# Kernel tuning notes

Measured on AMD Instinct MI355X. Metric: run time of the kernel, lower is better.

Reference implementation:

```python
import jax, jax.numpy as jnp
import numpy as np

HEADS = 4
ATTN_MODE = 'strided'
LOCAL_ATTN_CTX = 32
BLOCKSIZE = 32


def strided_transpose(x, n_ctx, local_attn_ctx):
    # [n, t, e] -> [n, bT_ctx, local, e] -> [n, local, bT_ctx, e] -> [n, t, e]
    bT_ctx = n_ctx // local_attn_ctx
    n, t, e = x.shape
    x = x.reshape(n, bT_ctx, local_attn_ctx, e)
    x = jnp.transpose(x, (0, 2, 1, 3))
    return x.reshape(n, t, e)


def setup_inputs() -> dict:
    key = jax.random.key(0)
    kq, kk, kv = jax.random.split(key, 3)
    shape = (2, 4096, 1024)
    return {
        'q': jax.random.normal(kq, shape, dtype=jnp.float32),
        'k': jax.random.normal(kk, shape, dtype=jnp.float32),
        'v': jax.random.normal(kv, shape, dtype=jnp.float32),
    }


def reference(q, k, v):
    n_ctx = q.shape[1]
    if ATTN_MODE == 'strided':
        bT_ctx = n_ctx // LOCAL_ATTN_CTX
        assert bT_ctx % BLOCKSIZE == 0
        q = strided_transpose(q, n_ctx, LOCAL_ATTN_CTX)
        k = strided_transpose(k, n_ctx, LOCAL_ATTN_CTX)
        v = strided_transpose(v, n_ctx, LOCAL_ATTN_CTX)
    n_state = q.shape[-1] // HEADS
    scale = 1.0 / np.sqrt(n_state)
    w = jnp.einsum('nte,nse->nts', q, k)            # [n, t, t] full scores
    w = jax.nn.softmax(w * scale, axis=-1)
    a = jnp.einsum('nts,nse->nte', w, v)
    if ATTN_MODE == 'strided':
        n, t, e = a.shape
        bT_ctx = n_ctx // LOCAL_ATTN_CTX
        a = a.reshape(n, LOCAL_ATTN_CTX, bT_ctx, e)
        a = jnp.transpose(a, (0, 2, 1, 3))
        a = a.reshape(n, t, e)
    return a
```

## Files before the change

kernel.cpp:

```cpp
#include <hip/hip_runtime.h>

using short8  = __attribute__((ext_vector_type(8))) short;
using ushort8 = __attribute__((ext_vector_type(8))) unsigned short;
using f32x4   = __attribute__((ext_vector_type(4))) float;

#define T 4096
#define E 1024
#define NB 2
#define BM 128
#define BN 128
#define BK 32
#define TILE_ELEMS (BM * BK)
#define TILE_A_W   (256 * BK)

__device__ __forceinline__ unsigned short f2bf(float f) {
    unsigned int u = __builtin_bit_cast(unsigned int, f);
    u = (u + 0x7FFFu + ((u >> 16) & 1u)) >> 16;
    return (unsigned short)u;
}

__device__ __forceinline__ void gld16(const unsigned short* g, unsigned short* l) {
    __builtin_amdgcn_global_load_lds(
        (__attribute__((address_space(1))) void*)g,
        (__attribute__((address_space(3))) void*)l, 16, 0, 0);
}

__device__ __forceinline__ void do_cvt(const float* __restrict__ src,
                                       unsigned short* __restrict__ dst, int blk) {
    size_t i = ((size_t)blk * 256 + threadIdx.x) * 8;
    float4 f0 = *(const float4*)(src + i);
    float4 f1 = *(const float4*)(src + i + 4);
    ushort8 u;
    u[0]=f2bf(f0.x); u[1]=f2bf(f0.y); u[2]=f2bf(f0.z); u[3]=f2bf(f0.w);
    u[4]=f2bf(f1.x); u[5]=f2bf(f1.y); u[6]=f2bf(f1.z); u[7]=f2bf(f1.w);
    *(ushort8*)(dst + i) = u;
}

__device__ __forceinline__ void do_vt(const float* __restrict__ v,
                                      unsigned short* __restrict__ vt, int id,
                                      float (*tile)[65]) {
    int b   = id / (64 * 16);
    int rem = id % (64 * 16);
    int t0  = (rem / 16) * 64;
    int e0  = (rem % 16) * 64;
    int tid = threadIdx.x;
    int r   = tid >> 2;
    int c0  = (tid & 3) * 16;
    const float* src = v + ((size_t)(b * T + t0 + r)) * E + e0 + c0;
    #pragma unroll
    for (int i = 0; i < 4; i++) {
        float4 f = *(const float4*)(src + i * 4);
        tile[r][c0 + i*4 + 0] = f.x;
        tile[r][c0 + i*4 + 1] = f.y;
        tile[r][c0 + i*4 + 2] = f.z;
        tile[r][c0 + i*4 + 3] = f.w;
    }
    __syncthreads();
    int er = tid >> 2;
    #pragma unroll
    for (int ch = 0; ch < 2; ch++) {
        int tl = (tid & 3) * 16 + ch * 8;
        ushort8 u;
        #pragma unroll
        for (int j = 0; j < 8; j++) u[j] = f2bf(tile[tl + j][er]);
        *(ushort8*)(vt + ((size_t)(b * E + e0 + er)) * T + t0 + tl) = u;
    }
}

__global__ __launch_bounds__(256) void prep(const float* __restrict__ q,
                                            const float* __restrict__ k,
                                            const float* __restrict__ v,
                                            unsigned short* __restrict__ qb,
                                            unsigned short* __restrict__ kb,
                                            unsigned short* __restrict__ vt,
                                            float* __restrict__ lsum) {
    __shared__ float tile[64][65];
    int bid = blockIdx.x;
    if (bid < 4096)        do_cvt(q, qb, bid);
    else if (bid < 8192)   do_cvt(k, kb, bid - 4096);
    else if (bid < 10240)  do_vt(v, vt, bid - 8192, tile);
    else                   lsum[(bid - 10240) * 256 + threadIdx.x] = 0.0f;
}

__global__ __launch_bounds__(256) void prologue(const float* __restrict__ q,
                                                const float* __restrict__ k,
                                                unsigned short* __restrict__ qb,
                                                unsigned short* __restrict__ kb,
                                                float* __restrict__ lsum) {
    int bid = blockIdx.x;
    if (bid < 4096)      do_cvt(q, qb, bid);
    else if (bid < 8192) do_cvt(k, kb, bid - 4096);
    else                 lsum[(bid - 8192) * 256 + threadIdx.x] = 0.0f;
}
__global__ __launch_bounds__(256) void v_transpose(const float* __restrict__ v,
                                                   unsigned short* __restrict__ vt) {
    __shared__ float tile[64][65];
    do_vt(v, vt, blockIdx.x, tile);
}

template <int KITERS, int NBUF>
__device__ __forceinline__ void gemm_core(const unsigned short* Abase, int apitch,
                                          const unsigned short* Bbase, int bpitch,
                                          unsigned short* ldsA, unsigned short* ldsB,
                                          int tid, f32x4 (&acc)[4][4]) {
    constexpr int D = NBUF - 1;
    const int lane = tid & 63, wave = tid >> 6;
    const int l15 = lane & 15, kq = lane >> 4;
    const int wm = (wave & 1) * 64, wn = (wave >> 1) * 64;

    const unsigned short* ga[2];
    const unsigned short* gb[2];
    int lo[2];
    #pragma unroll
    for (int i = 0; i < 2; i++) {
        int p = i * 256 + tid;
        int r = p >> 2;
        int kqw = (p & 3) ^ ((p >> 3) & 3);
        ga[i] = Abase + (size_t)r * apitch + kqw * 8;
        gb[i] = Bbase + (size_t)r * bpitch + kqw * 8;
        lo[i] = (i * 256 + wave * 64) * 8;
    }
    int aoff[4], boff[4];
    #pragma unroll
    for (int mi = 0; mi < 4; mi++) {
        int r = wm + mi * 16 + l15;
        aoff[mi] = (r * 4 + (kq ^ ((r >> 1) & 3))) * 8;
        int rn = wn + mi * 16 + l15;
        boff[mi] = (rn * 4 + (kq ^ ((rn >> 1) & 3))) * 8;
    }

    #pragma unroll
    for (int i = 0; i < D; i++) {
        gld16(ga[0] + i * BK, ldsA + i * TILE_ELEMS + lo[0]);
        gld16(ga[1] + i * BK, ldsA + i * TILE_ELEMS + lo[1]);
        gld16(gb[0] + i * BK, ldsB + i * TILE_ELEMS + lo[0]);
        gld16(gb[1] + i * BK, ldsB + i * TILE_ELEMS + lo[1]);
    }

    int cbuf = 0, pbuf = D, pkt = D;
    for (int kt = 0; kt < KITERS; kt++) {
        asm volatile("s_barrier" ::: "memory");
        gld16(ga[0] + pkt * BK, ldsA + pbuf * TILE_ELEMS + lo[0]);
        gld16(ga[1] + pkt * BK, ldsA + pbuf * TILE_ELEMS + lo[1]);
        gld16(gb[0] + pkt * BK, ldsB + pbuf * TILE_ELEMS + lo[0]);
        gld16(gb[1] + pkt * BK, ldsB + pbuf * TILE_ELEMS + lo[1]);
        if constexpr (D == 1) asm volatile("s_waitcnt vmcnt(4)" ::: "memory");
        else                  asm volatile("s_waitcnt vmcnt(8)" ::: "memory");
        asm volatile("s_barrier" ::: "memory");

        const unsigned short* A = ldsA + cbuf * TILE_ELEMS;
        const unsigned short* B = ldsB + cbuf * TILE_ELEMS;
        short8 af[4], bf[4];
        #pragma unroll
        for (int i = 0; i < 4; i++) {
            af[i] = *(const short8*)(A + aoff[i]);
            bf[i] = *(const short8*)(B + boff[i]);
        }
        #pragma unroll
        for (int mi = 0; mi < 4; mi++)
            #pragma unroll
            for (int ni = 0; ni < 4; ni++)
                acc[mi][ni] = __builtin_amdgcn_mfma_f32_16x16x32_bf16(af[mi], bf[ni], acc[mi][ni], 0, 0, 0);

        if (++cbuf == NBUF) cbuf = 0;
        if (++pbuf == NBUF) pbuf = 0;
        if (++pkt == KITERS) pkt = 0;
    }
}

template <int KITERS>
__device__ __forceinline__ void gemm_core_wide(const unsigned short* Abase, int apitch,
                                               const unsigned short* Bbase, int bpitch,
                                               unsigned short* ldsA, unsigned short* ldsB,
                                               int tid, f32x4 (&acc)[4][4]) {
    const int lane = tid & 63, wave = tid >> 6;
    const int l15 = lane & 15, kq = lane >> 4;
    const int wm = (wave & 3) * 64, wn = (wave >> 2) * 64;

    const unsigned short* ga[2];
    int lao[2];
    #pragma unroll
    for (int i = 0; i < 2; i++) {
        int p = i * 512 + tid;
        int r = p >> 2;
        int kqw = (p & 3) ^ ((p >> 3) & 3);
        ga[i] = Abase + (size_t)r * apitch + kqw * 8;
        lao[i] = (i * 512 + wave * 64) * 8;
    }
    const unsigned short* gb;
    int lbo;
    {
        int p = tid;
        int r = p >> 2;
        int kqw = (p & 3) ^ ((p >> 3) & 3);
        gb = Bbase + (size_t)r * bpitch + kqw * 8;
        lbo = (wave * 64) * 8;
    }
    int aoff[4], boff[4];
    #pragma unroll
    for (int mi = 0; mi < 4; mi++) {
        int r = wm + mi * 16 + l15;
        aoff[mi] = (r * 4 + (kq ^ ((r >> 1) & 3))) * 8;
        int rn = wn + mi * 16 + l15;
        boff[mi] = (rn * 4 + (kq ^ ((rn >> 1) & 3))) * 8;
    }

    gld16(ga[0], ldsA + lao[0]);
    gld16(ga[1], ldsA + lao[1]);
    gld16(gb,    ldsB + lbo);

    int cbuf = 0;
    for (int kt = 0; kt < KITERS; kt++) {
        int nxt = (kt + 1 < KITERS) ? (kt + 1) : 0;
        int obuf = cbuf ^ 1;
        asm volatile("s_barrier" ::: "memory");
        gld16(ga[0] + nxt * BK, ldsA + obuf * TILE_A_W + lao[0]);
        gld16(ga[1] + nxt * BK, ldsA + obuf * TILE_A_W + lao[1]);
        gld16(gb    + nxt * BK, ldsB + obuf * TILE_ELEMS + lbo);
        asm volatile("s_waitcnt vmcnt(3)" ::: "memory");
        asm volatile("s_barrier" ::: "memory");

        const unsigned short* A = ldsA + cbuf * TILE_A_W;
        const unsigned short* B = ldsB + cbuf * TILE_ELEMS;
        short8 af[4], bf[4];
        #pragma unroll
        for (int i = 0; i < 4; i++) {
            af[i] = *(const short8*)(A + aoff[i]);
            bf[i] = *(const short8*)(B + boff[i]);
        }
        #pragma unroll
        for (int mi = 0; mi < 4; mi++)
            #pragma unroll
            for (int ni = 0; ni < 4; ni++)
                acc[mi][ni] = __builtin_amdgcn_mfma_f32_16x16x32_bf16(af[mi], bf[ni], acc[mi][ni], 0, 0, 0);

        cbuf = obuf;
    }
}

__global__ __launch_bounds__(512, 2) void pass1(const unsigned short* __restrict__ qb,
                                                const unsigned short* __restrict__ kb,
                                                unsigned short* __restrict__ P,
                                                float* __restrict__ lsum) {
    __shared__ unsigned short ldsA[2 * TILE_A_W];
    __shared__ unsigned short ldsB[2 * TILE_ELEMS];
    const int bx = blockIdx.x;
    const int x = bx & 7, j = bx >> 3;
    const int gm = x * 4 + (j & 3);
    const int nt = j >> 2;
    const int b = gm >> 4, mt = gm & 15;
    const int tid = threadIdx.x;

    f32x4 acc[4][4];
    #pragma unroll
    for (int i = 0; i < 4; i++)
        #pragma unroll
        for (int jj = 0; jj < 4; jj++) acc[i][jj] = {};

    gemm_core_wide<E / BK>(qb + ((size_t)b * T + mt * 256) * E, E,
                           kb + ((size_t)b * T + nt * BN) * E, E,
                           ldsA, ldsB, tid, acc);

    const int lane = tid & 63, wave = tid >> 6;
    const int wm = (wave & 3) * 64, wn = (wave >> 2) * 64;
    const int quad = lane >> 4, l15 = lane & 15;
    const float sl2 = 0.0625f * 1.44269504089f;
    const int col0 = nt * BN + wn + l15;

    #pragma unroll
    for (int mi = 0; mi < 4; mi++) {
        #pragma unroll
        for (int r = 0; r < 4; r++) {
            int row = mt * 256 + wm + mi * 16 + quad * 4 + r;
            size_t base = ((size_t)b * T + row) * T + col0;
            float s = 0.0f;
            #pragma unroll
            for (int ni = 0; ni < 4; ni++) {
                float p = exp2f(acc[mi][ni][r] * sl2 - 12.0f);
                P[base + ni * 16] = f2bf(p);
                s += p;
            }
            s += __shfl_xor(s, 1);
            s += __shfl_xor(s, 2);
            s += __shfl_xor(s, 4);
            s += __shfl_xor(s, 8);
            if (l15 == 0) atomicAdd(lsum + b * T + row, s);
        }
    }
}

__global__ __launch_bounds__(256, 2) void pass2(const unsigned short* __restrict__ P,
                                                const unsigned short* __restrict__ vt,
                                                const float* __restrict__ lsum,
                                                float* __restrict__ out) {
    __shared__ unsigned short ldsA[3 * TILE_ELEMS];
    __shared__ unsigned short ldsB[3 * TILE_ELEMS];
    const int bx = blockIdx.x;
    const int x = bx & 7, j = bx >> 3;
    const int gm = x * 8 + (j & 7);
    const int nt = j >> 3;
    const int b = gm >> 5, mt = gm & 31;
    const int tid = threadIdx.x;

    f32x4 acc[4][4];
    #pragma unroll
    for (int i = 0; i < 4; i++)
        #pragma unroll
        for (int jj = 0; jj < 4; jj++) acc[i][jj] = {};

    gemm_core<T / BK, 3>(P + ((size_t)b * T + mt * BM) * T, T,
                         vt + ((size_t)b * E + nt * BN) * T, T,
                         ldsA, ldsB, tid, acc);

    const int lane = tid & 63, wave = tid >> 6;
    const int wm = (wave & 1) * 64, wn = (wave >> 1) * 64;
    const int quad = lane >> 4, l15 = lane & 15;
    const int col0 = nt * BN + wn + l15;

    #pragma unroll
    for (int mi = 0; mi < 4; mi++) {
        #pragma unroll
        for (int r = 0; r < 4; r++) {
            int row = mt * BM + wm + mi * 16 + quad * 4 + r;
            float rl = 1.0f / lsum[b * T + row];
            size_t base = ((size_t)b * T + row) * E + col0;
            #pragma unroll
            for (int ni = 0; ni < 4; ni++)
                out[base + ni * 16] = acc[mi][ni][r] * rl;
        }
    }
}

extern "C" void kernel_launch(void* const* d_in, const int* in_sizes, int n_in,
                              void* d_out, int out_size, void* d_ws, size_t ws_size,
                              hipStream_t stream) {
    const float* q = (const float*)d_in[0];
    const float* k = (const float*)d_in[1];
    const float* v = (const float*)d_in[2];
    float* out = (float*)d_out;

    const size_t QK = (size_t)NB * T * E;
    const size_t PSZ = (size_t)NB * T * T;
    float* lsum = (float*)d_ws;
    unsigned short* qbw = (unsigned short*)((char*)d_ws + 32768);
    unsigned short* kbw = qbw + QK;
    unsigned short* Pw  = kbw + QK;

    const size_t full_need = 32768 + (3 * QK + PSZ) * sizeof(unsigned short);

    if (ws_size >= full_need) {
        unsigned short* vtw = Pw + PSZ;
        prep<<<10272, 256, 0, stream>>>(q, k, v, qbw, kbw, vtw, lsum);
        pass1<<<1024, 512, 0, stream>>>(qbw, kbw, Pw, lsum);
        pass2<<<NB * 32 * 8, 256, 0, stream>>>(Pw, vtw, lsum, out);
    } else {
        unsigned short* vtw = qbw;
        prologue<<<8224, 256, 0, stream>>>(q, k, qbw, kbw, lsum);
        pass1<<<1024, 512, 0, stream>>>(qbw, kbw, Pw, lsum);
        v_transpose<<<NB * 64 * 16, 256, 0, stream>>>(v, vtw);
        pass2<<<NB * 32 * 8, 256, 0, stream>>>(Pw, vtw, lsum, out);
    }
}
```

Before: 293.0 us.

## Enlarge GEMM tiles to 256x256 and 256x128 with triple-buffered split-phase pipelining

pass1 now computes a 256x256 score tile per 512-thread block, with each wave covering 128x64 in two half-steps. The B-tile loads are interleaved between those half-steps over a triple-buffered LDS ring, and MFMA sections are raised to higher priority with s_setprio. pass2 moves to 512-thread blocks with 256x128 output tiles and triple buffering, halving the grid sizes. The aim is more operand reuse per global load and better overlap of loads with MFMA. In exchange, per-thread accumulator registers and LDS use rise, which may cut occupancy, and the smaller grids leave fewer blocks to spread across CUs.

```diff
diff --git a/kernel.cpp b/kernel.cpp
--- a/kernel.cpp
+++ b/kernel.cpp
@@ -7,11 +7,7 @@
 #define T 4096
 #define E 1024
 #define NB 2
-#define BM 128
-#define BN 128
 #define BK 32
-#define TILE_ELEMS (BM * BK)
-#define TILE_A_W   (256 * BK)
 
 __device__ __forceinline__ unsigned short f2bf(float f) {
     unsigned int u = __builtin_bit_cast(unsigned int, f);
@@ -98,177 +94,105 @@
     do_vt(v, vt, blockIdx.x, tile);
 }
 
-template <int KITERS, int NBUF>
-__device__ __forceinline__ void gemm_core(const unsigned short* Abase, int apitch,
-                                          const unsigned short* Bbase, int bpitch,
-                                          unsigned short* ldsA, unsigned short* ldsB,
-                                          int tid, f32x4 (&acc)[4][4]) {
-    constexpr int D = NBUF - 1;
-    const int lane = tid & 63, wave = tid >> 6;
-    const int l15 = lane & 15, kq = lane >> 4;
-    const int wm = (wave & 1) * 64, wn = (wave >> 1) * 64;
-
-    const unsigned short* ga[2];
-    const unsigned short* gb[2];
-    int lo[2];
-    #pragma unroll
-    for (int i = 0; i < 2; i++) {
-        int p = i * 256 + tid;
-        int r = p >> 2;
-        int kqw = (p & 3) ^ ((p >> 3) & 3);
-        ga[i] = Abase + (size_t)r * apitch + kqw * 8;
-        gb[i] = Bbase + (size_t)r * bpitch + kqw * 8;
-        lo[i] = (i * 256 + wave * 64) * 8;
-    }
-    int aoff[4], boff[4];
-    #pragma unroll
-    for (int mi = 0; mi < 4; mi++) {
-        int r = wm + mi * 16 + l15;
-        aoff[mi] = (r * 4 + (kq ^ ((r >> 1) & 3))) * 8;
-        int rn = wn + mi * 16 + l15;
-        boff[mi] = (rn * 4 + (kq ^ ((rn >> 1) & 3))) * 8;
-    }
-
-    #pragma unroll
-    for (int i = 0; i < D; i++) {
-        gld16(ga[0] + i * BK, ldsA + i * TILE_ELEMS + lo[0]);
-        gld16(ga[1] + i * BK, ldsA + i * TILE_ELEMS + lo[1]);
-        gld16(gb[0] + i * BK, ldsB + i * TILE_ELEMS + lo[0]);
-        gld16(gb[1] + i * BK, ldsB + i * TILE_ELEMS + lo[1]);
-    }
-
-    int cbuf = 0, pbuf = D, pkt = D;
-    for (int kt = 0; kt < KITERS; kt++) {
-        asm volatile("s_barrier" ::: "memory");
-        gld16(ga[0] + pkt * BK, ldsA + pbuf * TILE_ELEMS + lo[0]);
-        gld16(ga[1] + pkt * BK, ldsA + pbuf * TILE_ELEMS + lo[1]);
-        gld16(gb[0] + pkt * BK, ldsB + pbuf * TILE_ELEMS + lo[0]);
-        gld16(gb[1] + pkt * BK, ldsB + pbuf * TILE_ELEMS + lo[1]);
-        if constexpr (D == 1) asm volatile("s_waitcnt vmcnt(4)" ::: "memory");
-        else                  asm volatile("s_waitcnt vmcnt(8)" ::: "memory");
-        asm volatile("s_barrier" ::: "memory");
-
-        const unsigned short* A = ldsA + cbuf * TILE_ELEMS;
-        const unsigned short* B = ldsB + cbuf * TILE_ELEMS;
-        short8 af[4], bf[4];
-        #pragma unroll
-        for (int i = 0; i < 4; i++) {
-            af[i] = *(const short8*)(A + aoff[i]);
-            bf[i] = *(const short8*)(B + boff[i]);
-        }
-        #pragma unroll
-        for (int mi = 0; mi < 4; mi++)
-            #pragma unroll
-            for (int ni = 0; ni < 4; ni++)
-                acc[mi][ni] = __builtin_amdgcn_mfma_f32_16x16x32_bf16(af[mi], bf[ni], acc[mi][ni], 0, 0, 0);
-
-        if (++cbuf == NBUF) cbuf = 0;
-        if (++pbuf == NBUF) pbuf = 0;
-        if (++pkt == KITERS) pkt = 0;
-    }
-}
-
-template <int KITERS>
-__device__ __forceinline__ void gemm_core_wide(const unsigned short* Abase, int apitch,
-                                               const unsigned short* Bbase, int bpitch,
-                                               unsigned short* ldsA, unsigned short* ldsB,
-                                               int tid, f32x4 (&acc)[4][4]) {
-    const int lane = tid & 63, wave = tid >> 6;
-    const int l15 = lane & 15, kq = lane >> 4;
-    const int wm = (wave & 3) * 64, wn = (wave >> 2) * 64;
-
-    const unsigned short* ga[2];
-    int lao[2];
-    #pragma unroll
-    for (int i = 0; i < 2; i++) {
-        int p = i * 512 + tid;
-        int r = p >> 2;
-        int kqw = (p & 3) ^ ((p >> 3) & 3);
-        ga[i] = Abase + (size_t)r * apitch + kqw * 8;
-        lao[i] = (i * 512 + wave * 64) * 8;
-    }
-    const unsigned short* gb;
-    int lbo;
-    {
-        int p = tid;
-        int r = p >> 2;
-        int kqw = (p & 3) ^ ((p >> 3) & 3);
-        gb = Bbase + (size_t)r * bpitch + kqw * 8;
-        lbo = (wave * 64) * 8;
-    }
-    int aoff[4], boff[4];
-    #pragma unroll
-    for (int mi = 0; mi < 4; mi++) {
-        int r = wm + mi * 16 + l15;
-        aoff[mi] = (r * 4 + (kq ^ ((r >> 1) & 3))) * 8;
-        int rn = wn + mi * 16 + l15;
-        boff[mi] = (rn * 4 + (kq ^ ((rn >> 1) & 3))) * 8;
-    }
-
-    gld16(ga[0], ldsA + lao[0]);
-    gld16(ga[1], ldsA + lao[1]);
-    gld16(gb,    ldsB + lbo);
-
-    int cbuf = 0;
-    for (int kt = 0; kt < KITERS; kt++) {
-        int nxt = (kt + 1 < KITERS) ? (kt + 1) : 0;
-        int obuf = cbuf ^ 1;
-        asm volatile("s_barrier" ::: "memory");
-        gld16(ga[0] + nxt * BK, ldsA + obuf * TILE_A_W + lao[0]);
-        gld16(ga[1] + nxt * BK, ldsA + obuf * TILE_A_W + lao[1]);
-        gld16(gb    + nxt * BK, ldsB + obuf * TILE_ELEMS + lbo);
-        asm volatile("s_waitcnt vmcnt(3)" ::: "memory");
-        asm volatile("s_barrier" ::: "memory");
-
-        const unsigned short* A = ldsA + cbuf * TILE_A_W;
-        const unsigned short* B = ldsB + cbuf * TILE_ELEMS;
-        short8 af[4], bf[4];
-        #pragma unroll
-        for (int i = 0; i < 4; i++) {
-            af[i] = *(const short8*)(A + aoff[i]);
-            bf[i] = *(const short8*)(B + boff[i]);
-        }
-        #pragma unroll
-        for (int mi = 0; mi < 4; mi++)
-            #pragma unroll
-            for (int ni = 0; ni < 4; ni++)
-                acc[mi][ni] = __builtin_amdgcn_mfma_f32_16x16x32_bf16(af[mi], bf[ni], acc[mi][ni], 0, 0, 0);
-
-        cbuf = obuf;
-    }
-}
-
 __global__ __launch_bounds__(512, 2) void pass1(const unsigned short* __restrict__ qb,
                                                 const unsigned short* __restrict__ kb,
                                                 unsigned short* __restrict__ P,
                                                 float* __restrict__ lsum) {
-    __shared__ unsigned short ldsA[2 * TILE_A_W];
-    __shared__ unsigned short ldsB[2 * TILE_ELEMS];
+    constexpr int TW = 256 * BK;
+    __shared__ unsigned short ldsA[3 * TW];
+    __shared__ unsigned short ldsB[3 * TW];
+
     const int bx = blockIdx.x;
     const int x = bx & 7, j = bx >> 3;
     const int gm = x * 4 + (j & 3);
     const int nt = j >> 2;
     const int b = gm >> 4, mt = gm & 15;
     const int tid = threadIdx.x;
-
-    f32x4 acc[4][4];
-    #pragma unroll
-    for (int i = 0; i < 4; i++)
+    const int lane = tid & 63, wave = tid >> 6;
+    const int l15 = lane & 15, kq = lane >> 4;
+    const int wm = (wave & 1) * 128, wn = (wave >> 1) * 64;
+
+    const unsigned short* Ab = qb + ((size_t)b * T + mt * 256) * E;
+    const unsigned short* Bb = kb + ((size_t)b * T + nt * 256) * E;
+
+    const unsigned short* ga[2]; const unsigned short* gb[2]; int lo[2];
+    #pragma unroll
+    for (int i = 0; i < 2; i++) {
+        int p = i * 512 + tid;
+        int r = p >> 2;
+        int qs = (p & 3) ^ ((p >> 3) & 3);
+        ga[i] = Ab + (size_t)r * E + qs * 8;
+        gb[i] = Bb + (size_t)r * E + qs * 8;
+        lo[i] = (i * 512 + wave * 64) * 8;
+    }
+    int aoff[8], boff[4];
+    #pragma unroll
+    for (int mi = 0; mi < 8; mi++) { int r = wm + mi * 16 + l15; aoff[mi] = (r * 4 + (kq ^ ((r >> 1) & 3))) * 8; }
+    #pragma unroll
+    for (int ni = 0; ni < 4; ni++) { int r = wn + ni * 16 + l15; boff[ni] = (r * 4 + (kq ^ ((r >> 1) & 3))) * 8; }
+
+    f32x4 acc[8][4];
+    #pragma unroll
+    for (int i = 0; i < 8; i++)
         #pragma unroll
         for (int jj = 0; jj < 4; jj++) acc[i][jj] = {};
 
-    gemm_core_wide<E / BK>(qb + ((size_t)b * T + mt * 256) * E, E,
-                           kb + ((size_t)b * T + nt * BN) * E, E,
-                           ldsA, ldsB, tid, acc);
-
-    const int lane = tid & 63, wave = tid >> 6;
-    const int wm = (wave & 3) * 64, wn = (wave >> 2) * 64;
-    const int quad = lane >> 4, l15 = lane & 15;
+    #pragma unroll
+    for (int t = 0; t < 2; t++) {
+        gld16(ga[0] + t * BK, ldsA + t * TW + lo[0]);
+        gld16(ga[1] + t * BK, ldsA + t * TW + lo[1]);
+        gld16(gb[0] + t * BK, ldsB + t * TW + lo[0]);
+        gld16(gb[1] + t * BK, ldsB + t * TW + lo[1]);
+    }
+
+    int c = 0, p2 = 2, pk = 2;
+    for (int kt = 0; kt < E / BK; kt++) {
+        gld16(ga[0] + pk * BK, ldsA + p2 * TW + lo[0]);
+        gld16(ga[1] + pk * BK, ldsA + p2 * TW + lo[1]);
+        asm volatile("s_waitcnt vmcnt(6)" ::: "memory");
+        asm volatile("s_barrier" ::: "memory");
+
+        const unsigned short* A = ldsA + c * TW;
+        const unsigned short* B = ldsB + c * TW;
+        short8 af[4], bf[4];
+        #pragma unroll
+        for (int i = 0; i < 4; i++) {
+            af[i] = *(const short8*)(A + aoff[i]);
+            bf[i] = *(const short8*)(B + boff[i]);
+        }
+        __builtin_amdgcn_s_setprio(1);
+        #pragma unroll
+        for (int mi = 0; mi < 4; mi++)
+            #pragma unroll
+            for (int ni = 0; ni < 4; ni++)
+                acc[mi][ni] = __builtin_amdgcn_mfma_f32_16x16x32_bf16(af[mi], bf[ni], acc[mi][ni], 0, 0, 0);
+        __builtin_amdgcn_s_setprio(0);
+        asm volatile("s_barrier" ::: "memory");
+
+        gld16(gb[0] + pk * BK, ldsB + p2 * TW + lo[0]);
+        gld16(gb[1] + pk * BK, ldsB + p2 * TW + lo[1]);
+        short8 af2[4];
+        #pragma unroll
+        for (int i = 0; i < 4; i++) af2[i] = *(const short8*)(A + aoff[4 + i]);
+        __builtin_amdgcn_s_setprio(1);
+        #pragma unroll
+        for (int mi = 0; mi < 4; mi++)
+            #pragma unroll
+            for (int ni = 0; ni < 4; ni++)
+                acc[4 + mi][ni] = __builtin_amdgcn_mfma_f32_16x16x32_bf16(af2[mi], bf[ni], acc[4 + mi][ni], 0, 0, 0);
+        __builtin_amdgcn_s_setprio(0);
+        asm volatile("s_barrier" ::: "memory");
+
+        if (++c == 3) c = 0;
+        if (++p2 == 3) p2 = 0;
+        if (++pk == E / BK) pk = 0;
+    }
+
+    const int quad = lane >> 4;
     const float sl2 = 0.0625f * 1.44269504089f;
-    const int col0 = nt * BN + wn + l15;
-
-    #pragma unroll
-    for (int mi = 0; mi < 4; mi++) {
+    const int col0 = nt * 256 + wn + l15;
+    #pragma unroll
+    for (int mi = 0; mi < 8; mi++) {
         #pragma unroll
         for (int r = 0; r < 4; r++) {
             int row = mt * 256 + wm + mi * 16 + quad * 4 + r;
@@ -289,18 +213,50 @@
     }
 }
 
-__global__ __launch_bounds__(256, 2) void pass2(const unsigned short* __restrict__ P,
+__global__ __launch_bounds__(512, 2) void pass2(const unsigned short* __restrict__ P,
                                                 const unsigned short* __restrict__ vt,
                                                 const float* __restrict__ lsum,
                                                 float* __restrict__ out) {
-    __shared__ unsigned short ldsA[3 * TILE_ELEMS];
-    __shared__ unsigned short ldsB[3 * TILE_ELEMS];
+    constexpr int TWA = 256 * BK;
+    constexpr int TWB = 128 * BK;
+    __shared__ unsigned short ldsA[3 * TWA];
+    __shared__ unsigned short ldsB[3 * TWB];
+
     const int bx = blockIdx.x;
     const int x = bx & 7, j = bx >> 3;
-    const int gm = x * 8 + (j & 7);
-    const int nt = j >> 3;
-    const int b = gm >> 5, mt = gm & 31;
+    const int gm = x * 4 + (j & 3);
+    const int nt = j >> 2;
+    const int b = gm >> 4, mt = gm & 15;
     const int tid = threadIdx.x;
+    const int lane = tid & 63, wave = tid >> 6;
+    const int l15 = lane & 15, kq = lane >> 4;
+    const int wm = (wave & 3) * 64, wn = (wave >> 2) * 64;
+
+    const unsigned short* Ab = P + ((size_t)b * T + mt * 256) * T;
+    const unsigned short* Bb = vt + ((size_t)b * E + nt * 128) * T;
+
+    const unsigned short* ga[2]; int lao[2];
+    #pragma unroll
+    for (int i = 0; i < 2; i++) {
+        int p = i * 512 + tid;
+        int r = p >> 2;
+        int qs = (p & 3) ^ ((p >> 3) & 3);
+        ga[i] = Ab + (size_t)r * T + qs * 8;
+        lao[i] = (i * 512 + wave * 64) * 8;
+    }
+    const unsigned short* gb; int lbo;
+    {
+        int p = tid;
+        int r = p >> 2;
+        int qs = (p & 3) ^ ((p >> 3) & 3);
+        gb = Bb + (size_t)r * T + qs * 8;
+        lbo = (wave * 64) * 8;
+    }
+    int aoff[4], boff[4];
+    #pragma unroll
+    for (int mi = 0; mi < 4; mi++) { int r = wm + mi * 16 + l15; aoff[mi] = (r * 4 + (kq ^ ((r >> 1) & 3))) * 8; }
+    #pragma unroll
+    for (int ni = 0; ni < 4; ni++) { int r = wn + ni * 16 + l15; boff[ni] = (r * 4 + (kq ^ ((r >> 1) & 3))) * 8; }
 
     f32x4 acc[4][4];
     #pragma unroll
@@ -308,20 +264,50 @@
         #pragma unroll
         for (int jj = 0; jj < 4; jj++) acc[i][jj] = {};
 
-    gemm_core<T / BK, 3>(P + ((size_t)b * T + mt * BM) * T, T,
-                         vt + ((size_t)b * E + nt * BN) * T, T,
-                         ldsA, ldsB, tid, acc);
-
-    const int lane = tid & 63, wave = tid >> 6;
-    const int wm = (wave & 1) * 64, wn = (wave >> 1) * 64;
-    const int quad = lane >> 4, l15 = lane & 15;
-    const int col0 = nt * BN + wn + l15;
-
+    #pragma unroll
+    for (int t = 0; t < 2; t++) {
+        gld16(ga[0] + t * BK, ldsA + t * TWA + lao[0]);
+        gld16(ga[1] + t * BK, ldsA + t * TWA + lao[1]);
+        gld16(gb    + t * BK, ldsB + t * TWB + lbo);
+    }
+
+    int c = 0, p2 = 2, pk = 2;
+    for (int kt = 0; kt < T / BK; kt++) {
+        gld16(ga[0] + pk * BK, ldsA + p2 * TWA + lao[0]);
+        gld16(ga[1] + pk * BK, ldsA + p2 * TWA + lao[1]);
+        gld16(gb    + pk * BK, ldsB + p2 * TWB + lbo);
+        asm volatile("s_waitcnt vmcnt(6)" ::: "memory");
+        asm volatile("s_barrier" ::: "memory");
+
+        const unsigned short* A = ldsA + c * TWA;
+        const unsigned short* B = ldsB + c * TWB;
+        short8 af[4], bf[4];
+        #pragma unroll
+        for (int i = 0; i < 4; i++) {
+            af[i] = *(const short8*)(A + aoff[i]);
+            bf[i] = *(const short8*)(B + boff[i]);
+        }
+        __builtin_amdgcn_s_setprio(1);
+        #pragma unroll
+        for (int mi = 0; mi < 4; mi++)
+            #pragma unroll
+            for (int ni = 0; ni < 4; ni++)
+                acc[mi][ni] = __builtin_amdgcn_mfma_f32_16x16x32_bf16(af[mi], bf[ni], acc[mi][ni], 0, 0, 0);
+        __builtin_amdgcn_s_setprio(0);
+        asm volatile("s_barrier" ::: "memory");
+
+        if (++c == 3) c = 0;
+        if (++p2 == 3) p2 = 0;
+        if (++pk == T / BK) pk = 0;
+    }
+
+    const int quad = lane >> 4;
+    const int col0 = nt * 128 + wn + l15;
     #pragma unroll
     for (int mi = 0; mi < 4; mi++) {
         #pragma unroll
         for (int r = 0; r < 4; r++) {
-            int row = mt * BM + wm + mi * 16 + quad * 4 + r;
+            int row = mt * 256 + wm + mi * 16 + quad * 4 + r;
             float rl = 1.0f / lsum[b * T + row];
             size_t base = ((size_t)b * T + row) * E + col0;
             #pragma unroll
@@ -351,13 +337,13 @@
     if (ws_size >= full_need) {
         unsigned short* vtw = Pw + PSZ;
         prep<<<10272, 256, 0, stream>>>(q, k, v, qbw, kbw, vtw, lsum);
-        pass1<<<1024, 512, 0, stream>>>(qbw, kbw, Pw, lsum);
-        pass2<<<NB * 32 * 8, 256, 0, stream>>>(Pw, vtw, lsum, out);
+        pass1<<<512, 512, 0, stream>>>(qbw, kbw, Pw, lsum);
+        pass2<<<256, 512, 0, stream>>>(Pw, vtw, lsum, out);
     } else {
         unsigned short* vtw = qbw;
         prologue<<<8224, 256, 0, stream>>>(q, k, qbw, kbw, lsum);
-        pass1<<<1024, 512, 0, stream>>>(qbw, kbw, Pw, lsum);
+        pass1<<<512, 512, 0, stream>>>(qbw, kbw, Pw, lsum);
         v_transpose<<<NB * 64 * 16, 256, 0, stream>>>(v, vtw);
-        pass2<<<NB * 32 * 8, 256, 0, stream>>>(Pw, vtw, lsum, out);
-    }
-}
+        pass2<<<256, 512, 0, stream>>>(Pw, vtw, lsum, out);
+    }
+}
```

Measured after the change: 329.9 us. 12.6% more time.

## Use BK=64 double-buffered GEMM core with 8-way swizzle for both passes

Applied to the files above, without the earlier changes.

Replaces the two GEMM cores (BK=32 triple-buffered and wide 256-row variant) with a single 128x128 tile core using a 64-deep K step, double buffering and an 8-chunk XOR swizzle. Pass1 shrinks from 256x128 tiles on 512 threads to 128x128 tiles on 256 threads, with a new block-to-tile mapping, and launches twice as many blocks. Halving the number of K iterations halves the barriers per unit of work and gives more MFMAs per sync. In exchange LDS use per block rises for pass1, and pass1 reloads the K operand more often because its tiles are smaller.

```diff
diff --git a/kernel.cpp b/kernel.cpp
--- a/kernel.cpp
+++ b/kernel.cpp
@@ -7,11 +7,6 @@
 #define T 4096
 #define E 1024
 #define NB 2
-#define BM 128
-#define BN 128
-#define BK 32
-#define TILE_ELEMS (BM * BK)
-#define TILE_A_W   (256 * BK)
 
 __device__ __forceinline__ unsigned short f2bf(float f) {
     unsigned int u = __builtin_bit_cast(unsigned int, f);
@@ -98,157 +93,87 @@
     do_vt(v, vt, blockIdx.x, tile);
 }
 
-template <int KITERS, int NBUF>
-__device__ __forceinline__ void gemm_core(const unsigned short* Abase, int apitch,
-                                          const unsigned short* Bbase, int bpitch,
-                                          unsigned short* ldsA, unsigned short* ldsB,
-                                          int tid, f32x4 (&acc)[4][4]) {
-    constexpr int D = NBUF - 1;
+template <int KITERS>
+__device__ __forceinline__ void gemm_core64(const unsigned short* Abase, int apitch,
+                                            const unsigned short* Bbase, int bpitch,
+                                            unsigned short* ldsA, unsigned short* ldsB,
+                                            int tid, f32x4 (&acc)[4][4]) {
+    constexpr int TILE64 = 128 * 64;
     const int lane = tid & 63, wave = tid >> 6;
     const int l15 = lane & 15, kq = lane >> 4;
     const int wm = (wave & 1) * 64, wn = (wave >> 1) * 64;
 
-    const unsigned short* ga[2];
-    const unsigned short* gb[2];
-    int lo[2];
-    #pragma unroll
-    for (int i = 0; i < 2; i++) {
+    int goA[4], goB[4], lo[4];
+    #pragma unroll
+    for (int i = 0; i < 4; i++) {
         int p = i * 256 + tid;
-        int r = p >> 2;
-        int kqw = (p & 3) ^ ((p >> 3) & 3);
-        ga[i] = Abase + (size_t)r * apitch + kqw * 8;
-        gb[i] = Bbase + (size_t)r * bpitch + kqw * 8;
+        int r = p >> 3, s = p & 7;
+        int sw = s ^ (r & 7);
+        goA[i] = r * apitch + sw * 8;
+        goB[i] = r * bpitch + sw * 8;
         lo[i] = (i * 256 + wave * 64) * 8;
     }
-    int aoff[4], boff[4];
+    int aoff[2][4], boff[2][4];
     #pragma unroll
     for (int mi = 0; mi < 4; mi++) {
         int r = wm + mi * 16 + l15;
-        aoff[mi] = (r * 4 + (kq ^ ((r >> 1) & 3))) * 8;
+        aoff[0][mi] = (r * 8 + (kq ^ (r & 7))) * 8;
+        aoff[1][mi] = (r * 8 + ((kq ^ 4) ^ (r & 7))) * 8;
         int rn = wn + mi * 16 + l15;
-        boff[mi] = (rn * 4 + (kq ^ ((rn >> 1) & 3))) * 8;
-    }
-
-    #pragma unroll
-    for (int i = 0; i < D; i++) {
-        gld16(ga[0] + i * BK, ldsA + i * TILE_ELEMS + lo[0]);
-        gld16(ga[1] + i * BK, ldsA + i * TILE_ELEMS + lo[1]);
-        gld16(gb[0] + i * BK, ldsB + i * TILE_ELEMS + lo[0]);
-        gld16(gb[1] + i * BK, ldsB + i * TILE_ELEMS + lo[1]);
-    }
-
-    int cbuf = 0, pbuf = D, pkt = D;
-    for (int kt = 0; kt < KITERS; kt++) {
-        asm volatile("s_barrier" ::: "memory");
-        gld16(ga[0] + pkt * BK, ldsA + pbuf * TILE_ELEMS + lo[0]);
-        gld16(ga[1] + pkt * BK, ldsA + pbuf * TILE_ELEMS + lo[1]);
-        gld16(gb[0] + pkt * BK, ldsB + pbuf * TILE_ELEMS + lo[0]);
-        gld16(gb[1] + pkt * BK, ldsB + pbuf * TILE_ELEMS + lo[1]);
-        if constexpr (D == 1) asm volatile("s_waitcnt vmcnt(4)" ::: "memory");
-        else                  asm volatile("s_waitcnt vmcnt(8)" ::: "memory");
-        asm volatile("s_barrier" ::: "memory");
-
-        const unsigned short* A = ldsA + cbuf * TILE_ELEMS;
-        const unsigned short* B = ldsB + cbuf * TILE_ELEMS;
-        short8 af[4], bf[4];
-        #pragma unroll
-        for (int i = 0; i < 4; i++) {
-            af[i] = *(const short8*)(A + aoff[i]);
-            bf[i] = *(const short8*)(B + boff[i]);
-        }
-        #pragma unroll
-        for (int mi = 0; mi < 4; mi++)
-            #pragma unroll
-            for (int ni = 0; ni < 4; ni++)
-                acc[mi][ni] = __builtin_amdgcn_mfma_f32_16x16x32_bf16(af[mi], bf[ni], acc[mi][ni], 0, 0, 0);
-
-        if (++cbuf == NBUF) cbuf = 0;
-        if (++pbuf == NBUF) pbuf = 0;
-        if (++pkt == KITERS) pkt = 0;
-    }
-}
-
-template <int KITERS>
-__device__ __forceinline__ void gemm_core_wide(const unsigned short* Abase, int apitch,
-                                               const unsigned short* Bbase, int bpitch,
-                                               unsigned short* ldsA, unsigned short* ldsB,
-                                               int tid, f32x4 (&acc)[4][4]) {
-    const int lane = tid & 63, wave = tid >> 6;
-    const int l15 = lane & 15, kq = lane >> 4;
-    const int wm = (wave & 3) * 64, wn = (wave >> 2) * 64;
-
-    const unsigned short* ga[2];
-    int lao[2];
-    #pragma unroll
-    for (int i = 0; i < 2; i++) {
-        int p = i * 512 + tid;
-        int r = p >> 2;
-        int kqw = (p & 3) ^ ((p >> 3) & 3);
-        ga[i] = Abase + (size_t)r * apitch + kqw * 8;
-        lao[i] = (i * 512 + wave * 64) * 8;
-    }
-    const unsigned short* gb;
-    int lbo;
-    {
-        int p = tid;
-        int r = p >> 2;
-        int kqw = (p & 3) ^ ((p >> 3) & 3);
-        gb = Bbase + (size_t)r * bpitch + kqw * 8;
-        lbo = (wave * 64) * 8;
-    }
-    int aoff[4], boff[4];
-    #pragma unroll
-    for (int mi = 0; mi < 4; mi++) {
-        int r = wm + mi * 16 + l15;
-        aoff[mi] = (r * 4 + (kq ^ ((r >> 1) & 3))) * 8;
-        int rn = wn + mi * 16 + l15;
-        boff[mi] = (rn * 4 + (kq ^ ((rn >> 1) & 3))) * 8;
-    }
-
-    gld16(ga[0], ldsA + lao[0]);
-    gld16(ga[1], ldsA + lao[1]);
-    gld16(gb,    ldsB + lbo);
+        boff[0][mi] = (rn * 8 + (kq ^ (rn & 7))) * 8;
+        boff[1][mi] = (rn * 8 + ((kq ^ 4) ^ (rn & 7))) * 8;
+    }
+
+    #pragma unroll
+    for (int i = 0; i < 4; i++) gld16(Abase + goA[i], ldsA + lo[i]);
+    #pragma unroll
+    for (int i = 0; i < 4; i++) gld16(Bbase + goB[i], ldsB + lo[i]);
 
     int cbuf = 0;
     for (int kt = 0; kt < KITERS; kt++) {
-        int nxt = (kt + 1 < KITERS) ? (kt + 1) : 0;
-        int obuf = cbuf ^ 1;
+        int pk = (kt + 1 < KITERS) ? (kt + 1) : 0;
+        int ob = cbuf ^ 1;
         asm volatile("s_barrier" ::: "memory");
-        gld16(ga[0] + nxt * BK, ldsA + obuf * TILE_A_W + lao[0]);
-        gld16(ga[1] + nxt * BK, ldsA + obuf * TILE_A_W + lao[1]);
-        gld16(gb    + nxt * BK, ldsB + obuf * TILE_ELEMS + lbo);
-        asm volatile("s_waitcnt vmcnt(3)" ::: "memory");
+        #pragma unroll
+        for (int i = 0; i < 4; i++) gld16(Abase + goA[i] + pk * 64, ldsA + ob * TILE64 + lo[i]);
+        #pragma unroll
+        for (int i = 0; i < 4; i++) gld16(Bbase + goB[i] + pk * 64, ldsB + ob * TILE64 + lo[i]);
+        asm volatile("s_waitcnt vmcnt(8)" ::: "memory");
         asm volatile("s_barrier" ::: "memory");
 
-        const unsigned short* A = ldsA + cbuf * TILE_A_W;
-        const unsigned short* B = ldsB + cbuf * TILE_ELEMS;
-        short8 af[4], bf[4];
-        #pragma unroll
-        for (int i = 0; i < 4; i++) {
-            af[i] = *(const short8*)(A + aoff[i]);
-            bf[i] = *(const short8*)(B + boff[i]);
+        const unsigned short* A = ldsA + cbuf * TILE64;
+        const unsigned short* B = ldsB + cbuf * TILE64;
+        #pragma unroll
+        for (int ks = 0; ks < 2; ks++) {
+            short8 af[4], bf[4];
+            #pragma unroll
+            for (int i = 0; i < 4; i++) {
+                af[i] = *(const short8*)(A + aoff[ks][i]);
+                bf[i] = *(const short8*)(B + boff[ks][i]);
+            }
+            #pragma unroll
+            for (int mi = 0; mi < 4; mi++)
+                #pragma unroll
+                for (int ni = 0; ni < 4; ni++)
+                    acc[mi][ni] = __builtin_amdgcn_mfma_f32_16x16x32_bf16(af[mi], bf[ni], acc[mi][ni], 0, 0, 0);
         }
-        #pragma unroll
-        for (int mi = 0; mi < 4; mi++)
-            #pragma unroll
-            for (int ni = 0; ni < 4; ni++)
-                acc[mi][ni] = __builtin_amdgcn_mfma_f32_16x16x32_bf16(af[mi], bf[ni], acc[mi][ni], 0, 0, 0);
-
-        cbuf = obuf;
-    }
-}
-
-__global__ __launch_bounds__(512, 2) void pass1(const unsigned short* __restrict__ qb,
+        cbuf = ob;
+    }
+}
+
+__global__ __launch_bounds__(256, 2) void pass1(const unsigned short* __restrict__ qb,
                                                 const unsigned short* __restrict__ kb,
                                                 unsigned short* __restrict__ P,
                                                 float* __restrict__ lsum) {
-    __shared__ unsigned short ldsA[2 * TILE_A_W];
-    __shared__ unsigned short ldsB[2 * TILE_ELEMS];
+    constexpr int TILE64 = 128 * 64;
+    __shared__ unsigned short ldsA[2 * TILE64];
+    __shared__ unsigned short ldsB[2 * TILE64];
+
     const int bx = blockIdx.x;
     const int x = bx & 7, j = bx >> 3;
-    const int gm = x * 4 + (j & 3);
-    const int nt = j >> 2;
-    const int b = gm >> 4, mt = gm & 15;
+    const int rt = x * 8 + (j >> 5);
+    const int nt = j & 31;
+    const int b = rt >> 5, mt = rt & 31;
     const int tid = threadIdx.x;
 
     f32x4 acc[4][4];
@@ -257,21 +182,21 @@
         #pragma unroll
         for (int jj = 0; jj < 4; jj++) acc[i][jj] = {};
 
-    gemm_core_wide<E / BK>(qb + ((size_t)b * T + mt * 256) * E, E,
-                           kb + ((size_t)b * T + nt * BN) * E, E,
-                           ldsA, ldsB, tid, acc);
+    gemm_core64<E / 64>(qb + ((size_t)b * T + mt * 128) * E, E,
+                        kb + ((size_t)b * T + nt * 128) * E, E,
+                        ldsA, ldsB, tid, acc);
 
     const int lane = tid & 63, wave = tid >> 6;
-    const int wm = (wave & 3) * 64, wn = (wave >> 2) * 64;
+    const int wm = (wave & 1) * 64, wn = (wave >> 1) * 64;
     const int quad = lane >> 4, l15 = lane & 15;
     const float sl2 = 0.0625f * 1.44269504089f;
-    const int col0 = nt * BN + wn + l15;
+    const int col0 = nt * 128 + wn + l15;
 
     #pragma unroll
     for (int mi = 0; mi < 4; mi++) {
         #pragma unroll
         for (int r = 0; r < 4; r++) {
-            int row = mt * 256 + wm + mi * 16 + quad * 4 + r;
+            int row = mt * 128 + wm + mi * 16 + quad * 4 + r;
             size_t base = ((size_t)b * T + row) * T + col0;
             float s = 0.0f;
             #pragma unroll
@@ -293,8 +218,10 @@
                                                 const unsigned short* __restrict__ vt,
                                                 const float* __restrict__ lsum,
                                                 float* __restrict__ out) {
-    __shared__ unsigned short ldsA[3 * TILE_ELEMS];
-    __shared__ unsigned short ldsB[3 * TILE_ELEMS];
+    constexpr int TILE64 = 128 * 64;
+    __shared__ unsigned short ldsA[2 * TILE64];
+    __shared__ unsigned short ldsB[2 * TILE64];
+
     const int bx = blockIdx.x;
     const int x = bx & 7, j = bx >> 3;
     const int gm = x * 8 + (j & 7);
@@ -308,20 +235,20 @@
         #pragma unroll
         for (int jj = 0; jj < 4; jj++) acc[i][jj] = {};
 
-    gemm_core<T / BK, 3>(P + ((size_t)b * T + mt * BM) * T, T,
-                         vt + ((size_t)b * E + nt * BN) * T, T,
-                         ldsA, ldsB, tid, acc);
+    gemm_core64<T / 64>(P + ((size_t)b * T + mt * 128) * T, T,
+                        vt + ((size_t)b * E + nt * 128) * T, T,
+                        ldsA, ldsB, tid, acc);
 
     const int lane = tid & 63, wave = tid >> 6;
     const int wm = (wave & 1) * 64, wn = (wave >> 1) * 64;
     const int quad = lane >> 4, l15 = lane & 15;
-    const int col0 = nt * BN + wn + l15;
+    const int col0 = nt * 128 + wn + l15;
 
     #pragma unroll
     for (int mi = 0; mi < 4; mi++) {
         #pragma unroll
         for (int r = 0; r < 4; r++) {
-            int row = mt * BM + wm + mi * 16 + quad * 4 + r;
+            int row = mt * 128 + wm + mi * 16 + quad * 4 + r;
             float rl = 1.0f / lsum[b * T + row];
             size_t base = ((size_t)b * T + row) * E + col0;
             #pragma unroll
@@ -351,13 +278,13 @@
     if (ws_size >= full_need) {
         unsigned short* vtw = Pw + PSZ;
         prep<<<10272, 256, 0, stream>>>(q, k, v, qbw, kbw, vtw, lsum);
-        pass1<<<1024, 512, 0, stream>>>(qbw, kbw, Pw, lsum);
-        pass2<<<NB * 32 * 8, 256, 0, stream>>>(Pw, vtw, lsum, out);
+        pass1<<<2048, 256, 0, stream>>>(qbw, kbw, Pw, lsum);
+        pass2<<<512, 256, 0, stream>>>(Pw, vtw, lsum, out);
     } else {
         unsigned short* vtw = qbw;
         prologue<<<8224, 256, 0, stream>>>(q, k, qbw, kbw, lsum);
-        pass1<<<1024, 512, 0, stream>>>(qbw, kbw, Pw, lsum);
+        pass1<<<2048, 256, 0, stream>>>(qbw, kbw, Pw, lsum);
         v_transpose<<<NB * 64 * 16, 256, 0, stream>>>(v, vtw);
-        pass2<<<NB * 32 * 8, 256, 0, stream>>>(Pw, vtw, lsum, out);
-    }
-}
+        pass2<<<512, 256, 0, stream>>>(Pw, vtw, lsum, out);
+    }
+}
```

Measured after the change: 313.0 us. 1.07x slower.
